# Performance work log

Hardware: AMD Instinct MI355X
Metric: run time of the kernel (lower is better)

Reference implementation:

```python
import jax, jax.numpy as jnp
import numpy as np

EPS = 1e-5

def _ln(x, g, b):
    m = jnp.mean(x, axis=-1, keepdims=True)
    v = jnp.mean((x - m) ** 2, axis=-1, keepdims=True)
    return (x - m) / jnp.sqrt(v + EPS) * g + b

B, SX, SY = 2, 2048, 2048
XD, YD, P, H, MULT = 1024, 1024, 64, 16, 4

def setup_inputs() -> dict:
    key = jax.random.key(0)
    ks = jax.random.split(key, 20)
    s = lambda fan: 1.0 / np.sqrt(fan)
    return {
        "x": jax.random.normal(ks[0], (B, SX, XD), jnp.float32),
        "y": jax.random.normal(ks[1], (B, SY, YD), jnp.float32),
        "gx_gamma": jnp.ones((XD,), jnp.float32),
        "gx_beta": jnp.zeros((XD,), jnp.float32),
        "gy_gamma": jnp.ones((YD,), jnp.float32),
        "gy_beta": jnp.zeros((YD,), jnp.float32),
        "Wq": jax.random.uniform(ks[2], (H, XD, P), jnp.float32, -s(XD), s(XD)),
        "bq": jax.random.uniform(ks[3], (H, P), jnp.float32, -s(XD), s(XD)),
        "Wk": jax.random.uniform(ks[4], (H, YD, P), jnp.float32, -s(YD), s(YD)),
        "bk": jax.random.uniform(ks[5], (H, P), jnp.float32, -s(YD), s(YD)),
        "Wv": jax.random.uniform(ks[6], (H, YD, P), jnp.float32, -s(YD), s(YD)),
        "bv": jax.random.uniform(ks[7], (H, P), jnp.float32, -s(YD), s(YD)),
        "Wo": jax.random.uniform(ks[8], (H * P, XD), jnp.float32, -s(H * P), s(H * P)),
        "bo": jax.random.uniform(ks[9], (XD,), jnp.float32, -s(H * P), s(H * P)),
        "gd_gamma": jnp.ones((XD,), jnp.float32),
        "gd_beta": jnp.zeros((XD,), jnp.float32),
        "W1": jax.random.uniform(ks[10], (XD, MULT * XD), jnp.float32, -s(XD), s(XD)),
        "b1": jax.random.uniform(ks[11], (MULT * XD,), jnp.float32, -s(XD), s(XD)),
        "W2": jax.random.uniform(ks[12], (MULT * XD, XD), jnp.float32, -s(MULT * XD), s(MULT * XD)),
        "b2": jax.random.uniform(ks[13], (XD,), jnp.float32, -s(MULT * XD), s(MULT * XD)),
        "mask": 1,
    }

def reference(x, y, gx_gamma, gx_beta, gy_gamma, gy_beta, Wq, bq, Wk, bk, Wv, bv,
              Wo, bo, gd_gamma, gd_beta, W1, b1, W2, b2, mask):
    xn = _ln(x, gx_gamma, gx_beta)
    yn = _ln(y, gy_gamma, gy_beta)
    # batched per-head projections: [B,S,D] x [H,D,P] -> [B,H,S,P]
    q = jnp.einsum('bsd,hdp->bhsp', xn, Wq) + bq[None, :, None, :]
    k = jnp.einsum('btd,hdp->bhtp', yn, Wk) + bk[None, :, None, :]
    v = jnp.einsum('btd,hdp->bhtp', yn, Wv) + bv[None, :, None, :]
    scores = jnp.einsum('bhsp,bhtp->bhst', q, k) * (1.0 / jnp.sqrt(jnp.float32(P)))
    attn = jax.nn.softmax(scores, axis=-1)
    if mask:
        # post-softmax strictly-upper-triangular mask (torch.triu diagonal=1)
        tri = jnp.triu(jnp.ones((SX, SY), attn.dtype), k=1)
        attn = attn * tri
    o = jnp.einsum('bhst,bhtp->bhsp', attn, v)          # [B,H,S,P]
    o = o.transpose(0, 2, 1, 3).reshape(B, SX, H * P)    # concat heads
    x2 = x + o @ Wo + bo
    h = jax.nn.gelu(_ln(x2, gd_gamma, gd_beta) @ W1 + b1, approximate=False)
    return x2 + h @ W2 + b2
```

## Files before the change

### kernel.cpp

```cpp
#include <hip/hip_runtime.h>
#include <hip/hip_bf16.h>
#include <math.h>

typedef __bf16 bf16_t;
typedef __bf16 bf16x8 __attribute__((ext_vector_type(8)));
typedef __bf16 bf16x4 __attribute__((ext_vector_type(4)));
typedef float f32x4 __attribute__((ext_vector_type(4)));

#define QSCALE 0.18033688011112042f

static __device__ __forceinline__ f32x4 mfma16(bf16x8 a, bf16x8 b, f32x4 c) {
  return __builtin_amdgcn_mfma_f32_16x16x32_bf16(a, b, c, 0, 0, 0);
}

static __device__ __forceinline__ float gelu_f(float x) {
  return 0.5f * x * (1.0f + erff(x * 0.70710678118654752440f));
}

static __device__ __forceinline__ float exp2_fast(float x) {
  float r;
  asm("v_exp_f32 %0, %1" : "=v"(r) : "v"(x));
  return r;
}

typedef __attribute__((address_space(1))) const void as1_void;
typedef __attribute__((address_space(3))) void as3_void;
static __device__ __forceinline__ void gload16(const void* g, void* s) {
  __builtin_amdgcn_global_load_lds((as1_void*)g, (as3_void*)s, 16, 0, 0);
}

static __device__ __forceinline__ long hmi(int row, int col) {
  return ((((long)(row >> 11) * 16 + (col >> 6)) * 2048) + (row & 2047)) * 64 + (col & 63);
}

__global__ __launch_bounds__(256) void prep_all(
    const float* __restrict__ Wq, const float* __restrict__ Wk, const float* __restrict__ Wv,
    const float* __restrict__ Wo, const float* __restrict__ W1, const float* __restrict__ W2,
    bf16_t* __restrict__ WqkvT, bf16_t* __restrict__ WoT, bf16_t* __restrict__ W1T,
    bf16_t* __restrict__ W2T, const float* __restrict__ x, const float* __restrict__ y,
    const float* __restrict__ gx, const float* __restrict__ bex, const float* __restrict__ gy,
    const float* __restrict__ bey, bf16_t* __restrict__ xn, bf16_t* __restrict__ yn) {
  const int bid = blockIdx.x;
  if (bid >= 3072) {
    const int lrow = bid - 3072;
    const float* in = lrow < 4096 ? x : y;
    const float* g = lrow < 4096 ? gx : gy;
    const float* be = lrow < 4096 ? bex : bey;
    bf16_t* out = lrow < 4096 ? xn : yn;
    const int row = lrow & 4095;
    const int t = threadIdx.x;
    const float4 xv = ((const float4*)(in + (long)row * 1024))[t];
    float s1 = xv.x + xv.y + xv.z + xv.w;
    float s2 = xv.x * xv.x + xv.y * xv.y + xv.z * xv.z + xv.w * xv.w;
#pragma unroll
    for (int m = 1; m < 64; m <<= 1) {
      s1 += __shfl_xor(s1, m);
      s2 += __shfl_xor(s2, m);
    }
    __shared__ float r1[4], r2[4];
    if ((t & 63) == 0) { r1[t >> 6] = s1; r2[t >> 6] = s2; }
    __syncthreads();
    s1 = r1[0] + r1[1] + r1[2] + r1[3];
    s2 = r2[0] + r2[1] + r2[2] + r2[3];
    const float mean = s1 * (1.0f / 1024.0f);
    float var = s2 * (1.0f / 1024.0f) - mean * mean;
    const float rstd = rsqrtf(fmaxf(var, 0.0f) + 1e-5f);
    const float4 gv = ((const float4*)g)[t];
    const float4 bv = ((const float4*)be)[t];
    bf16x4 o;
    o[0] = (bf16_t)((xv.x - mean) * rstd * gv.x + bv.x);
    o[1] = (bf16_t)((xv.y - mean) * rstd * gv.y + bv.y);
    o[2] = (bf16_t)((xv.z - mean) * rstd * gv.z + bv.z);
    o[3] = (bf16_t)((xv.w - mean) * rstd * gv.w + bv.w);
    *(bf16x4*)(out + (long)row * 1024 + t * 4) = o;
    return;
  }
  const float* inp;
  bf16_t* outp;
  int istride, ostride, i0, j0;
  if (bid < 768) {
    const int wsel = bid >> 8, rem = bid & 255;
    const int h = rem >> 4, xt = rem & 15;
    const float* W = wsel == 0 ? Wq : (wsel == 1 ? Wk : Wv);
    inp = W + h * 65536;
    outp = WqkvT + (long)wsel * 1048576 + h * 65536;
    istride = 64; ostride = 1024; i0 = xt * 64; j0 = 0;
  } else if (bid < 1024) {
    const int rem = bid - 768;
    inp = Wo; outp = WoT; istride = 1024; ostride = 1024;
    i0 = (rem & 15) * 64; j0 = (rem >> 4) * 64;
  } else if (bid < 2048) {
    const int rem = bid - 1024;
    inp = W1; outp = W1T; istride = 4096; ostride = 1024;
    i0 = (rem & 15) * 64; j0 = (rem >> 4) * 64;
  } else {
    const int rem = bid - 2048;
    inp = W2; outp = W2T; istride = 1024; ostride = 4096;
    i0 = (rem >> 4) * 64; j0 = (rem & 15) * 64;
  }
  __shared__ bf16_t tile[64][65];
  const int r = threadIdx.x >> 2, cs = (threadIdx.x & 3) * 16;
#pragma unroll
  for (int jj = 0; jj < 16; jj++)
    tile[cs + jj][r] = (bf16_t)inp[(long)(i0 + r) * istride + j0 + cs + jj];
  __syncthreads();
#pragma unroll
  for (int jj = 0; jj < 16; jj++)
    outp[(long)(j0 + r) * ostride + i0 + cs + jj] = tile[r][cs + jj];
}

__global__ __launch_bounds__(256) void ln_kernel(const float* __restrict__ in,
                                                 const float* __restrict__ g,
                                                 const float* __restrict__ be,
                                                 bf16_t* __restrict__ out) {
  const int row = blockIdx.x, t = threadIdx.x;
  const float4 xv = ((const float4*)(in + (long)row * 1024))[t];
  float s1 = xv.x + xv.y + xv.z + xv.w;
  float s2 = xv.x * xv.x + xv.y * xv.y + xv.z * xv.z + xv.w * xv.w;
#pragma unroll
  for (int m = 1; m < 64; m <<= 1) {
    s1 += __shfl_xor(s1, m);
    s2 += __shfl_xor(s2, m);
  }
  __shared__ float r1[4], r2[4];
  if ((t & 63) == 0) { r1[t >> 6] = s1; r2[t >> 6] = s2; }
  __syncthreads();
  s1 = r1[0] + r1[1] + r1[2] + r1[3];
  s2 = r2[0] + r2[1] + r2[2] + r2[3];
  const float mean = s1 * (1.0f / 1024.0f);
  float var = s2 * (1.0f / 1024.0f) - mean * mean;
  const float rstd = rsqrtf(fmaxf(var, 0.0f) + 1e-5f);
  const float4 gv = ((const float4*)g)[t];
  const float4 bv = ((const float4*)be)[t];
  bf16x4 o;
  o[0] = (bf16_t)((xv.x - mean) * rstd * gv.x + bv.x);
  o[1] = (bf16_t)((xv.y - mean) * rstd * gv.y + bv.y);
  o[2] = (bf16_t)((xv.z - mean) * rstd * gv.z + bv.z);
  o[3] = (bf16_t)((xv.w - mean) * rstd * gv.w + bv.w);
  *(bf16x4*)(out + (long)row * 1024 + t * 4) = o;
}

template <int EPI, int BN, int RW>
__global__ __launch_bounds__(256) void gemm32(const bf16_t* __restrict__ A,
                                              const bf16_t* __restrict__ A2,
                                              const bf16_t* __restrict__ Bt,
                                              const float* __restrict__ bias,
                                              const float* __restrict__ biasB,
                                              const float* __restrict__ biasC,
                                              bf16_t* __restrict__ aux,
                                              void* __restrict__ Cout,
                                              int M, int N, int K) {
  constexpr int NF = BN / 32;
  constexpr int NBI = BN / 64;
  __shared__ bf16_t a_lds[3][128 * 32];
  __shared__ bf16_t b_lds[3][BN * 32];
  const int tid = threadIdx.x, l = tid & 63, w = tid >> 6;
  const int wr = w >> 1, wc = w & 1;
  const int nwg = gridDim.x * gridDim.y;
  const int orig = blockIdx.y * gridDim.x + blockIdx.x;
  const int cpx = nwg >> 3;
  const int xcd = orig & 7, ii = orig >> 3;
  const int rpr = gridDim.x / RW;
  const int bx = (xcd % rpr) * RW + (ii % RW);
  const int by = (xcd / rpr) * (cpx / RW) + (ii / RW);
  const int m0 = by * 128, n0 = bx * BN;
  const bf16_t* Ause = (EPI == 5 && n0 >= 1024) ? A2 : A;
  const int lr = l & 15, lg = l >> 4;
  long a_src[2];
  int a_dst[2];
#pragma unroll
  for (int i = 0; i < 2; i++) {
    const int row = i * 64 + (tid >> 2);
    const int sc = ((tid & 3) ^ ((row >> 1) & 3)) * 8;
    a_src[i] = (long)(m0 + row) * K + sc;
    a_dst[i] = (i * 64 + w * 16) * 32;
  }
  long b_src[NBI];
#pragma unroll
  for (int i = 0; i < NBI; i++) {
    const int row = i * 64 + (tid >> 2);
    const int sc = ((tid & 3) ^ ((row >> 1) & 3)) * 8;
    b_src[i] = (long)(n0 + row) * K + sc;
  }
  const int nk = K >> 5;
  f32x4 acc[4][NF] = {};
#pragma unroll
  for (int tt = 0; tt < 2; tt++) {
#pragma unroll
    for (int i = 0; i < 2; i++) gload16(Ause + a_src[i] + tt * 32, &a_lds[tt][a_dst[i]]);
#pragma unroll
    for (int i = 0; i < NBI; i++) gload16(Bt + b_src[i] + tt * 32, &b_lds[tt][a_dst[i]]);
  }
  int cu = 0;
  for (int t = 0; t < nk; t++) {
    if (t + 1 < nk) asm volatile("s_waitcnt vmcnt(4)" ::: "memory");
    else            asm volatile("s_waitcnt vmcnt(0)" ::: "memory");
    __builtin_amdgcn_s_barrier();
    __builtin_amdgcn_sched_barrier(0);
    if (t + 2 < nk) {
      const long k0 = (long)(t + 2) * 32;
      const int nb = cu >= 1 ? cu - 1 : 2;
#pragma unroll
      for (int i = 0; i < 2; i++) gload16(Ause + a_src[i] + k0, &a_lds[nb][a_dst[i]]);
#pragma unroll
      for (int i = 0; i < NBI; i++) gload16(Bt + b_src[i] + k0, &b_lds[nb][a_dst[i]]);
    }
    const char* ab = (const char*)&a_lds[cu][0];
    const char* bb = (const char*)&b_lds[cu][0];
    bf16x8 af[4], bfr[NF];
#pragma unroll
    for (int m = 0; m < 4; m++) {
      const int row = wr * 64 + m * 16 + lr;
      af[m] = *(const bf16x8*)(ab + row * 64 + 16 * (lg ^ ((row >> 1) & 3)));
    }
#pragma unroll
    for (int n = 0; n < NF; n++) {
      const int row = wc * (BN / 2) + n * 16 + lr;
      bfr[n] = *(const bf16x8*)(bb + row * 64 + 16 * (lg ^ ((row >> 1) & 3)));
    }
    __builtin_amdgcn_s_setprio(1);
#pragma unroll
    for (int m = 0; m < 4; m++)
#pragma unroll
      for (int n = 0; n < NF; n++) acc[m][n] = mfma16(af[m], bfr[n], acc[m][n]);
    __builtin_amdgcn_s_setprio(0);
    cu = cu < 2 ? cu + 1 : 0;
  }
#pragma unroll
  for (int m = 0; m < 4; m++)
#pragma unroll
    for (int n = 0; n < NF; n++) {
      const int row_b = m0 + wr * 64 + m * 16 + (l >> 4) * 4;
      const int col = n0 + wc * (BN / 2) + n * 16 + lr;
      if (EPI == 2) {
        const float bia = bias[col];
#pragma unroll
        for (int r = 0; r < 4; r++) {
          const long idx = (long)(row_b + r) * N + col;
          ((bf16_t*)Cout)[idx] = (bf16_t)gelu_f(acc[m][n][r] + bia);
        }
      } else if (EPI == 5) {
        if (col < 1024) {
          const float bia = bias[col];
#pragma unroll
          for (int r = 0; r < 4; r++)
            ((bf16_t*)Cout)[hmi(row_b + r, col)] = (bf16_t)((acc[m][n][r] + bia) * QSCALE);
        } else if (col < 2048) {
          const float bia = biasB[col - 1024];
#pragma unroll
          for (int r = 0; r < 4; r++)
            ((bf16_t*)Cout + 4194304)[hmi(row_b + r, col - 1024)] =
                (bf16_t)(acc[m][n][r] + bia);
        } else {
          const int vcol = col - 2048;
          const float bia = biasC[vcol];
          bf16x4 vv;
#pragma unroll
          for (int r = 0; r < 4; r++) vv[r] = (bf16_t)(acc[m][n][r] + bia);
          const int bb2 = row_b >> 11, tt = row_b & 2047;
          *(bf16x4*)&aux[(((long)(bb2 << 4) + (vcol >> 6)) * 64 + (vcol & 63)) * 2048 + tt] = vv;
        }
      }
    }
}

template <int EPI, int BN>
__global__ __launch_bounds__(256) void gemm64(const bf16_t* __restrict__ A,
                                              const bf16_t* __restrict__ Bt,
                                              const float* __restrict__ bias,
                                              const float* __restrict__ res,
                                              void* __restrict__ Cout,
                                              int M, int N, int K) {
  constexpr int NF = BN / 32;
  constexpr int NBI = BN / 32;
  __shared__ bf16_t a_lds[2][128 * 64];
  __shared__ bf16_t b_lds[2][BN * 64];
  const int tid = threadIdx.x, l = tid & 63, w = tid >> 6;
  const int wr = w >> 1, wc = w & 1;
  const int nwg = gridDim.x * gridDim.y;
  const int orig = blockIdx.y * gridDim.x + blockIdx.x;
  const int lid = (orig & 7) * (nwg >> 3) + (orig >> 3);
  const int bx = lid % gridDim.x, by = lid / gridDim.x;
  const int m0 = by * 128, n0 = bx * BN;
  const int lr = l & 15, lg = l >> 4;
  long a_src[4];
  int ldst[4];
#pragma unroll
  for (int i = 0; i < 4; i++) {
    const int row = i * 32 + w * 8 + (l >> 3);
    const int sc = ((l & 7) ^ (row & 7)) * 8;
    a_src[i] = (long)(m0 + row) * K + sc;
    ldst[i] = (i * 32 + w * 8) * 64;
  }
  long b_src[NBI];
#pragma unroll
  for (int i = 0; i < NBI; i++) {
    const int row = i * 32 + w * 8 + (l >> 3);
    const int sc = ((l & 7) ^ (row & 7)) * 8;
    b_src[i] = (long)(n0 + row) * K + sc;
  }
  const int nk = K >> 6;
  f32x4 acc[4][NF] = {};
#pragma unroll
  for (int i = 0; i < 4; i++) gload16(A + a_src[i], &a_lds[0][ldst[i]]);
#pragma unroll
  for (int i = 0; i < NBI; i++) gload16(Bt + b_src[i], &b_lds[0][ldst[i]]);
  __syncthreads();
  const int sw = (lr & 7) << 4;
  int cur = 0;
  for (int t = 0; t < nk; t++) {
    if (t + 1 < nk) {
      const long k0 = (long)(t + 1) * 64;
#pragma unroll
      for (int i = 0; i < 4; i++) gload16(A + a_src[i] + k0, &a_lds[cur ^ 1][ldst[i]]);
#pragma unroll
      for (int i = 0; i < NBI; i++) gload16(Bt + b_src[i] + k0, &b_lds[cur ^ 1][ldst[i]]);
    }
    const char* ab = (const char*)&a_lds[cur][0];
    const char* bb = (const char*)&b_lds[cur][0];
    bf16x8 af[4][2], bfr[NF][2];
#pragma unroll
    for (int m = 0; m < 4; m++) {
      const int rb = (wr * 64 + m * 16 + lr) * 128;
      af[m][0] = *(const bf16x8*)(ab + rb + ((16 * lg) ^ sw));
      af[m][1] = *(const bf16x8*)(ab + rb + ((16 * lg + 64) ^ sw));
    }
#pragma unroll
    for (int n = 0; n < NF; n++) {
      const int rb = (wc * (BN / 2) + n * 16 + lr) * 128;
      bfr[n][0] = *(const bf16x8*)(bb + rb + ((16 * lg) ^ sw));
      bfr[n][1] = *(const bf16x8*)(bb + rb + ((16 * lg + 64) ^ sw));
    }
    __builtin_amdgcn_s_setprio(1);
#pragma unroll
    for (int kk = 0; kk < 2; kk++)
#pragma unroll
      for (int m = 0; m < 4; m++)
#pragma unroll
        for (int n = 0; n < NF; n++)
          acc[m][n] = mfma16(af[m][kk], bfr[n][kk], acc[m][n]);
    __builtin_amdgcn_s_setprio(0);
    __syncthreads();
    cur ^= 1;
  }
#pragma unroll
  for (int m = 0; m < 4; m++)
#pragma unroll
    for (int n = 0; n < NF; n++) {
      const int row_b = m0 + wr * 64 + m * 16 + (l >> 4) * 4;
      const int col = n0 + wc * (BN / 2) + n * 16 + lr;
      const float bia = bias[col];
#pragma unroll
      for (int r = 0; r < 4; r++) {
        const long idx = (long)(row_b + r) * N + col;
        ((float*)Cout)[idx] = acc[m][n][r] + bia + res[idx];
      }
    }
}

__global__ __launch_bounds__(256) void attn_kernel(const bf16_t* __restrict__ qhm,
                                                   const bf16_t* __restrict__ khm,
                                                   const bf16_t* __restrict__ vtg,
                                                   bf16_t* __restrict__ og,
                                                   const int* __restrict__ maskp) {
  const int T = 2048, HP = 1024;
  __shared__ bf16_t k_lds[2][64 * 64];
  __shared__ bf16_t vt_lds[2][64 * 64];
  __shared__ bf16_t p_lds[4 * 32 * 72];
  const int bh = blockIdx.x, b = bh >> 4, h = bh & 15;
  const int q0 = blockIdx.y * 128;
  const int tid = threadIdx.x, l = tid & 63, w = tid >> 6;
  const int lr = l & 15, lg = l >> 4, lg4 = lg * 4;
  const int srow0 = q0 + w * 32 + lr;
  const bf16_t* kbase = khm + (long)bh * T * 64;
  const bf16_t* vbase = vtg + (long)bh * 64 * T;
  bf16x8 qf[2][2];
#pragma unroll
  for (int g = 0; g < 2; g++) {
    const bf16_t* qr = qhm + ((long)bh * 2048 + srow0 + g * 16) * 64 + lg * 8;
    qf[g][0] = *(const bf16x8*)qr;
    qf[g][1] = *(const bf16x8*)(qr + 32);
  }
  bf16_t* pl = &p_lds[w * 32 * 72];
  float lpart[2] = {0.0f, 0.0f};
  f32x4 oat[4][2] = {};

  const int swz = (lr & 7) << 4;
  const int fo0 = lr * 128 + ((16 * lg) ^ swz);
  const int fo1 = lr * 128 + ((64 + 16 * lg) ^ swz);

  const bool do_mask = (maskp[0] != 0);
  const int nM = do_mask ? (q0 >> 6) : 0;
  const int nt = T >> 6;

  const int sch = l & 7, srow8 = l >> 3;
  int cur = 0;
  {
    const bool needV = (nM == 0);
#pragma unroll
    for (int i = 0; i < 2; i++) {
      const int row = (i * 4 + w) * 8 + srow8;
      const int sc = (sch ^ (row & 7)) * 8;
      gload16(kbase + (long)row * 64 + sc, &k_lds[0][(i * 4 + w) * 512]);
      if (needV) gload16(vbase + (long)row * 2048 + 0 + sc, &vt_lds[0][(i * 4 + w) * 512]);
    }
  }
  __syncthreads();

  for (int t = 0; t < nt; t++) {
    const int t0 = t << 6;
    const int mode = (t < nM) ? 0 : ((do_mask && t < nM + 2) ? 1 : 2);
    if (t + 1 < nt) {
      const int t1 = (t + 1) << 6;
      const bool needV = (t + 1) >= nM;
#pragma unroll
      for (int i = 0; i < 2; i++) {
        const int row = (i * 4 + w) * 8 + srow8;
        const int sc = (sch ^ (row & 7)) * 8;
        gload16(kbase + (long)(t1 + row) * 64 + sc, &k_lds[cur ^ 1][(i * 4 + w) * 512]);
        if (needV)
          gload16(vbase + (long)row * 2048 + t1 + sc, &vt_lds[cur ^ 1][(i * 4 + w) * 512]);
      }
    }
    const char* kb = (const char*)&k_lds[cur][0];
    f32x4 sacc[4][2];
    __builtin_amdgcn_s_setprio(1);
#pragma unroll
    for (int n = 0; n < 4; n++) {
      bf16x8 kf0 = *(const bf16x8*)(kb + n * 2048 + fo0);
      bf16x8 kf1 = *(const bf16x8*)(kb + n * 2048 + fo1);
#pragma unroll
      for (int g = 0; g < 2; g++) {
        f32x4 z = {0.0f, 0.0f, 0.0f, 0.0f};
        z = mfma16(kf0, qf[g][0], z);
        sacc[n][g] = mfma16(kf1, qf[g][1], z);
      }
    }
    __builtin_amdgcn_s_setprio(0);
    float pv[2][4][4];
#pragma unroll
    for (int g = 0; g < 2; g++) {
      float psn[4];
#pragma unroll
      for (int n = 0; n < 4; n++) {
        pv[g][n][0] = exp2_fast(sacc[n][g][0]);
        pv[g][n][1] = exp2_fast(sacc[n][g][1]);
        pv[g][n][2] = exp2_fast(sacc[n][g][2]);
        pv[g][n][3] = exp2_fast(sacc[n][g][3]);
        psn[n] = (pv[g][n][0] + pv[g][n][1]) + (pv[g][n][2] + pv[g][n][3]);
      }
      lpart[g] += (psn[0] + psn[1]) + (psn[2] + psn[3]);
    }
    if (mode > 0) {
#pragma unroll
      for (int g = 0; g < 2; g++)
#pragma unroll
        for (int n = 0; n < 4; n++) {
          bf16x4 pk;
#pragma unroll
          for (int r = 0; r < 4; r++) {
            float v = pv[g][n][r];
            if (mode == 1 && (t0 + n * 16 + lg4 + r) <= srow0 + g * 16) v = 0.0f;
            pk[r] = (bf16_t)v;
          }
          *(bf16x4*)&pl[(g * 16 + lr) * 72 + n * 16 + lg4] = pk;
        }
      const char* vtb = (const char*)&vt_lds[cur][0];
      __builtin_amdgcn_s_setprio(1);
#pragma unroll
      for (int kk = 0; kk < 2; kk++) {
        bf16x8 pb0 = *(bf16x8*)&pl[lr * 72 + kk * 32 + lg * 8];
        bf16x8 pb1 = *(bf16x8*)&pl[(16 + lr) * 72 + kk * 32 + lg * 8];
        const int fkk = lr * 128 + ((kk * 64 + 16 * lg) ^ swz);
#pragma unroll
        for (int np = 0; np < 4; np++) {
          bf16x8 vtf = *(const bf16x8*)(vtb + np * 2048 + fkk);
          oat[np][0] = mfma16(vtf, pb0, oat[np][0]);
          oat[np][1] = mfma16(vtf, pb1, oat[np][1]);
        }
      }
      __builtin_amdgcn_s_setprio(0);
    }
    __syncthreads();
    cur ^= 1;
  }
  float inv[2];
#pragma unroll
  for (int g = 0; g < 2; g++) {
    float lsum = lpart[g];
    lsum += __shfl_xor(lsum, 16);
    lsum += __shfl_xor(lsum, 32);
    inv[g] = 1.0f / lsum;
  }
#pragma unroll
  for (int g = 0; g < 2; g++)
#pragma unroll
    for (int np = 0; np < 4; np++) {
      bf16x4 o4;
#pragma unroll
      for (int r = 0; r < 4; r++) o4[r] = (bf16_t)(oat[np][g][r] * inv[g]);
      *(bf16x4*)&pl[(g * 16 + lr) * 72 + np * 16 + lg4] = o4;
    }
  const int es = l >> 2, ec = (l & 3) * 16;
#pragma unroll
  for (int g = 0; g < 2; g++) {
    bf16x8 o0 = *(bf16x8*)&pl[(g * 16 + es) * 72 + ec];
    bf16x8 o1 = *(bf16x8*)&pl[(g * 16 + es) * 72 + ec + 8];
    bf16_t* orow = og + (long)(b * 2048 + q0 + w * 32 + g * 16 + es) * HP + h * 64 + ec;
    *(bf16x8*)&orow[0] = o0;
    *(bf16x8*)&orow[8] = o1;
  }
}

extern "C" void kernel_launch(void* const* d_in, const int* in_sizes, int n_in,
                              void* d_out, int out_size, void* d_ws, size_t ws_size,
                              hipStream_t stream) {
  const float* x = (const float*)d_in[0];
  const float* y = (const float*)d_in[1];
  const float* gxg = (const float*)d_in[2];
  const float* gxb = (const float*)d_in[3];
  const float* gyg = (const float*)d_in[4];
  const float* gyb = (const float*)d_in[5];
  const float* Wq = (const float*)d_in[6];
  const float* bq = (const float*)d_in[7];
  const float* Wk = (const float*)d_in[8];
  const float* bk = (const float*)d_in[9];
  const float* Wv = (const float*)d_in[10];
  const float* bv = (const float*)d_in[11];
  const float* Wo = (const float*)d_in[12];
  const float* bo = (const float*)d_in[13];
  const float* gdg = (const float*)d_in[14];
  const float* gdb = (const float*)d_in[15];
  const float* W1 = (const float*)d_in[16];
  const float* b1 = (const float*)d_in[17];
  const float* W2 = (const float*)d_in[18];
  const float* b2 = (const float*)d_in[19];
  const int* maskp = (const int*)d_in[20];
  float* out = (float*)d_out;

  char* ws = (char*)d_ws;
  const long MB = 1024 * 1024;
  bf16_t* xn = (bf16_t*)(ws + 0);
  bf16_t* yn = (bf16_t*)(ws + 8 * MB);
  bf16_t* WqkvT = (bf16_t*)(ws + 16 * MB);
  bf16_t* WoT = (bf16_t*)(ws + 22 * MB);
  bf16_t* W1T = (bf16_t*)(ws + 24 * MB);
  bf16_t* W2T = (bf16_t*)(ws + 32 * MB);
  bf16_t* qhm = (bf16_t*)(ws + 40 * MB);
  bf16_t* vTb = (bf16_t*)(ws + 64 * MB);
  bf16_t* ob = (bf16_t*)(ws + 0);
  bf16_t* xd = (bf16_t*)(ws + 8 * MB);
  bf16_t* hb = (bf16_t*)(ws + 40 * MB);
  bf16_t* khm = qhm + 4194304;

  prep_all<<<11264, 256, 0, stream>>>(Wq, Wk, Wv, Wo, W1, W2, WqkvT, WoT, W1T, W2T, x, y, gxg,
                                      gxb, gyg, gyb, xn, yn);
  gemm32<5, 128, 12><<<dim3(24, 32), 256, 0, stream>>>(xn, yn, WqkvT, bq, bk, bv, vTb, qhm,
                                                       4096, 3072, 1024);
  attn_kernel<<<dim3(32, 16), 256, 0, stream>>>(qhm, khm, vTb, ob, maskp);
  gemm64<1, 64><<<dim3(16, 32), 256, 0, stream>>>(ob, WoT, bo, x, out, 4096, 1024, 1024);
  ln_kernel<<<4096, 256, 0, stream>>>(out, gdg, gdb, xd);
  gemm32<2, 128, 16><<<dim3(32, 32), 256, 0, stream>>>(xd, nullptr, W1T, b1, nullptr, nullptr,
                                                       nullptr, hb, 4096, 4096, 1024);
  gemm64<1, 64><<<dim3(16, 32), 256, 0, stream>>>(hb, W2T, b2, out, out, 4096, 1024, 4096);
}
```

Measured before the change: 249.5 us.

## Add 256x256-tile 8-wave GEMM kernel for the W1 GELU projection

```diff
diff --git a/kernel.cpp b/kernel.cpp
--- a/kernel.cpp
+++ b/kernel.cpp
@@ -138,6 +138,114 @@
   o[2] = (bf16_t)((xv.z - mean) * rstd * gv.z + bv.z);
   o[3] = (bf16_t)((xv.w - mean) * rstd * gv.w + bv.w);
   *(bf16x4*)(out + (long)row * 1024 + t * 4) = o;
+}
+
+template <int EPI>
+__global__ __launch_bounds__(512, 2) void gemm256(const bf16_t* __restrict__ A,
+                                                  const bf16_t* __restrict__ Bt,
+                                                  const float* __restrict__ bias,
+                                                  void* __restrict__ Cout,
+                                                  int M, int N, int K) {
+  __shared__ bf16_t a_l[2][2][256 * 32];
+  __shared__ bf16_t b_l[2][2][256 * 32];
+  const int tid = threadIdx.x, l = tid & 63, wid = tid >> 6;
+  const int wr = wid >> 2, wc = wid & 3;
+  const int lr = l & 15, lg = l >> 4;
+  const int orig = blockIdx.y * gridDim.x + blockIdx.x;
+  const int xcd = orig & 7, ii = orig >> 3;
+  const int bx = (xcd & 3) * 4 + (ii & 3);
+  const int by = (xcd >> 2) * 8 + (ii >> 2);
+  const int m0 = by * 256, n0 = bx * 256;
+  const int sr0 = tid >> 2, sr1 = 128 + (tid >> 2);
+  const int sch2 = ((tid & 3) ^ ((tid >> 3) & 3)) * 8;
+  const int sl0 = sr0 * 32 + (tid & 3) * 8;
+  const int sl1 = sr1 * 32 + (tid & 3) * 8;
+#define STG_A(bufi, kki, kcol)                                        \
+  do {                                                                \
+    gload16(A + (long)(m0 + sr0) * K + (kcol) + sch2, &a_l[bufi][kki][sl0]); \
+    gload16(A + (long)(m0 + sr1) * K + (kcol) + sch2, &a_l[bufi][kki][sl1]); \
+  } while (0)
+#define STG_B(bufi, kki, kcol)                                        \
+  do {                                                                \
+    gload16(Bt + (long)(n0 + sr0) * K + (kcol) + sch2, &b_l[bufi][kki][sl0]); \
+    gload16(Bt + (long)(n0 + sr1) * K + (kcol) + sch2, &b_l[bufi][kki][sl1]); \
+  } while (0)
+  const int ch = (lg ^ ((lr >> 1) & 3)) * 8;
+  const int nt = K >> 6;
+  f32x4 acc[8][4] = {};
+  bf16x8 af[8], bf2[2];
+  STG_A(0, 0, 0); STG_B(0, 0, 0);
+  STG_A(0, 1, 32); STG_B(0, 1, 32);
+  STG_A(1, 0, 64); STG_B(1, 0, 64);
+  asm volatile("s_waitcnt vmcnt(8)" ::: "memory");
+  __builtin_amdgcn_s_barrier();
+  for (int t = 0; t < nt; t++) {
+    const int buf = t & 1, nbuf = buf ^ 1;
+    const long kc = (long)t * 64;
+#define RD_A(kki)                                                      \
+  _Pragma("unroll") for (int m = 0; m < 8; m++) af[m] =                \
+      *(const bf16x8*)&a_l[buf][kki][(wr * 128 + m * 16 + lr) * 32 + ch];
+#define RD_B(kki, nh)                                                  \
+  _Pragma("unroll") for (int j = 0; j < 2; j++) bf2[j] =               \
+      *(const bf16x8*)&b_l[buf][kki][(wc * 64 + ((nh)*2 + j) * 16 + lr) * 32 + ch];
+#define MM(nh)                                                         \
+  __builtin_amdgcn_s_setprio(1);                                       \
+  _Pragma("unroll") for (int m = 0; m < 8; m++) {                      \
+    acc[m][(nh)*2 + 0] = mfma16(af[m], bf2[0], acc[m][(nh)*2 + 0]);    \
+    acc[m][(nh)*2 + 1] = mfma16(af[m], bf2[1], acc[m][(nh)*2 + 1]);    \
+  }                                                                    \
+  __builtin_amdgcn_s_setprio(0);
+    RD_A(0); RD_B(0, 0);
+    if (t + 1 < nt) { STG_A(nbuf, 1, kc + 96); }
+    __builtin_amdgcn_s_barrier();
+    asm volatile("s_waitcnt lgkmcnt(0)" ::: "memory");
+    __builtin_amdgcn_sched_barrier(0);
+    MM(0);
+    __builtin_amdgcn_s_barrier();
+    RD_B(0, 1);
+    if (t + 1 < nt) { STG_B(nbuf, 1, kc + 96); }
+    if (t + 1 < nt) asm volatile("s_waitcnt vmcnt(8)" ::: "memory");
+    else            asm volatile("s_waitcnt vmcnt(0)" ::: "memory");
+    __builtin_amdgcn_s_barrier();
+    asm volatile("s_waitcnt lgkmcnt(0)" ::: "memory");
+    __builtin_amdgcn_sched_barrier(0);
+    MM(1);
+    __builtin_amdgcn_s_barrier();
+    RD_A(1); RD_B(1, 0);
+    if (t + 2 < nt) { STG_A(buf, 0, kc + 128); }
+    __builtin_amdgcn_s_barrier();
+    asm volatile("s_waitcnt lgkmcnt(0)" ::: "memory");
+    __builtin_amdgcn_sched_barrier(0);
+    MM(0);
+    __builtin_amdgcn_s_barrier();
+    RD_B(1, 1);
+    if (t + 2 < nt) { STG_B(buf, 0, kc + 128); }
+    if (t + 2 < nt)      asm volatile("s_waitcnt vmcnt(8)" ::: "memory");
+    else if (t + 1 < nt) asm volatile("s_waitcnt vmcnt(4)" ::: "memory");
+    __builtin_amdgcn_s_barrier();
+    asm volatile("s_waitcnt lgkmcnt(0)" ::: "memory");
+    __builtin_amdgcn_sched_barrier(0);
+    MM(1);
+    __builtin_amdgcn_s_barrier();
+  }
+#undef RD_A
+#undef RD_B
+#undef MM
+#undef STG_A
+#undef STG_B
+#pragma unroll
+  for (int m = 0; m < 8; m++)
+#pragma unroll
+    for (int n = 0; n < 4; n++) {
+      const int row_b = m0 + wr * 128 + m * 16 + lg * 4;
+      const int col = n0 + wc * 64 + n * 16 + lr;
+      const float bia = bias[col];
+#pragma unroll
+      for (int r = 0; r < 4; r++) {
+        const long idx = (long)(row_b + r) * N + col;
+        if (EPI == 2) ((bf16_t*)Cout)[idx] = (bf16_t)gelu_f(acc[m][n][r] + bia);
+      }
+    }
 }
 
 template <int EPI, int BN, int RW>
@@ -560,7 +668,6 @@
   attn_kernel<<<dim3(32, 16), 256, 0, stream>>>(qhm, khm, vTb, ob, maskp);
   gemm64<1, 64><<<dim3(16, 32), 256, 0, stream>>>(ob, WoT, bo, x, out, 4096, 1024, 1024);
   ln_kernel<<<4096, 256, 0, stream>>>(out, gdg, gdb, xd);
-  gemm32<2, 128, 16><<<dim3(32, 32), 256, 0, stream>>>(xd, nullptr, W1T, b1, nullptr, nullptr,
-                                                       nullptr, hb, 4096, 4096, 1024);
+  gemm256<2><<<dim3(16, 16), 512, 0, stream>>>(xd, W1T, b1, hb, 4096, 4096, 1024);
   gemm64<1, 64><<<dim3(16, 32), 256, 0, stream>>>(hb, W2T, b2, out, out, 4096, 1024, 4096);
 }
```

Measured after the change: 239.3 us. -4.1%, faster.
